# Optimization experiments

Measured on AMD Instinct MI355X. Metric: run time of the kernel, lower is better.

## Reference

```python
import jax, jax.numpy as jnp
import numpy as np

N = 100000        # nodes
E = 1600000       # edges (avg degree 16)
D1, D2 = 512, 256 # omic feature dims
H = 64            # hidden_dim
C = 4             # num_classes


def setup_inputs() -> dict:
    key = jax.random.key(0)
    ks = jax.random.split(key, 13)
    s = 0.05  # param scale
    return {
        "x_omic1": jax.random.normal(ks[0], (N, D1), dtype=jnp.float32),
        "x_omic2": jax.random.normal(ks[1], (N, D2), dtype=jnp.float32),
        "edge_index": jax.random.randint(ks[2], (2, E), 0, N, dtype=jnp.int32),
        # GCNConv weights/biases, branch 1 (omic1)
        "W1a": jax.random.normal(ks[3], (D1, H), dtype=jnp.float32) * s,
        "b1a": jnp.zeros((H,), dtype=jnp.float32),
        "W2a": jax.random.normal(ks[4], (H, H), dtype=jnp.float32) * s,
        "b2a": jnp.zeros((H,), dtype=jnp.float32),
        # branch 2 (omic2)
        "W1b": jax.random.normal(ks[5], (D2, H), dtype=jnp.float32) * s,
        "b1b": jnp.zeros((H,), dtype=jnp.float32),
        "W2b": jax.random.normal(ks[6], (H, H), dtype=jnp.float32) * s,
        "b2b": jnp.zeros((H,), dtype=jnp.float32),
        # final classifier
        "Wfc": jax.random.normal(ks[7], (2 * H, C), dtype=jnp.float32) * s,
        "bfc": jnp.zeros((C,), dtype=jnp.float32),
    }


def reference(x_omic1, x_omic2, edge_index, W1a, b1a, W2a, b2a,
              W1b, b1b, W2b, b2b, Wfc, bfc):
    n = x_omic1.shape[0]
    # GCN normalization with self-loops: A_hat = A + I, norm = d^-1/2 d^-1/2
    loop = jnp.arange(n, dtype=edge_index.dtype)
    src = jnp.concatenate([edge_index[0], loop])
    dst = jnp.concatenate([edge_index[1], loop])
    deg = jax.ops.segment_sum(jnp.ones_like(src, dtype=x_omic1.dtype), dst,
                              num_segments=n)
    dinv = jnp.where(deg > 0, jax.lax.rsqrt(jnp.maximum(deg, 1.0)), 0.0)
    norm = dinv[src] * dinv[dst]  # [E+N]

    def gcn(x, W, b):
        h = x @ W                              # dense linear [n, H]
        msg = h[src] * norm[:, None]           # gather + scale
        return jax.ops.segment_sum(msg, dst, num_segments=n) + b

    # dropout is identity in eval mode
    x1 = jax.nn.elu(gcn(x_omic1, W1a, b1a))
    x1 = jax.nn.elu(gcn(x1, W2a, b2a))
    x2 = jax.nn.elu(gcn(x_omic2, W1b, b1b))
    x2 = jax.nn.elu(gcn(x2, W2b, b2b))
    x = jnp.concatenate([x1, x2], axis=1)      # [n, 2H]
    return x @ Wfc + bfc
```

## Files before the change

kernel.cpp:

```cpp
#include <hip/hip_runtime.h>
#include <hip/hip_bf16.h>
#include <math.h>


#define H 64
#define BCAP 16384

static inline int ceil_div(int a, int b) { return (a + b - 1) / b; }

typedef __attribute__((ext_vector_type(8))) short short8_t;
typedef __attribute__((ext_vector_type(4))) float f32x4;

__device__ inline unsigned short f2bf_rne(float f) {
    unsigned u = __float_as_uint(f);
    u += 0x7fffu + ((u >> 16) & 1u);
    return (unsigned short)(u >> 16);
}
__device__ inline unsigned pk_bf(float a, float b) {
    return (unsigned)f2bf_rne(a) | ((unsigned)f2bf_rne(b) << 16);
}
__device__ inline float2 bf2x(unsigned w) {
    float2 r;
    r.x = __uint_as_float(w << 16);
    r.y = __uint_as_float(w & 0xffff0000u);
    return r;
}
union V8 { uint4 u4; unsigned u[4]; short8_t s; };

__global__ __launch_bounds__(256) void bucket_scatter_kernel(
        const int* __restrict__ src, const int* __restrict__ dst,
        int* __restrict__ cursor, unsigned* __restrict__ bucketed,
        int E, int nbkt) {
    __shared__ int lcnt[512];
    __shared__ int lbase[512];
    const int t = threadIdx.x;
    for (int b = t; b < nbkt; b += 256) lcnt[b] = 0;
    __syncthreads();

    unsigned val[8];
    int bkt[8], lpos[8];
    const int e0 = blockIdx.x * 2048;
#pragma unroll
    for (int k = 0; k < 8; ++k) {
        int e = e0 + k * 256 + t;
        bkt[k] = -1;
        if (e < E) {
            int s = src[e];
            int d = dst[e];
            int b = d >> 8;
            val[k] = (unsigned)s | ((unsigned)(d & 255) << 17);
            bkt[k] = b;
            lpos[k] = atomicAdd(&lcnt[b], 1);
        }
    }
    __syncthreads();
    for (int b = t; b < nbkt; b += 256) {
        int c = lcnt[b];
        lbase[b] = c > 0 ? atomicAdd(&cursor[b], c) : 0;
    }
    __syncthreads();
#pragma unroll
    for (int k = 0; k < 8; ++k) {
        if (bkt[k] >= 0) {
            int p = lbase[bkt[k]] + lpos[k];
            if (p < BCAP)
                bucketed[(size_t)bkt[k] * BCAP + p] = val[k];
        }
    }
}

__global__ __launch_bounds__(256) void bucket_csr_kernel(
        const unsigned* __restrict__ bucketed, const int* __restrict__ cursor,
        int* __restrict__ csr_src, int* __restrict__ row_ptr,
        float* __restrict__ dinv, int N, int E) {
    __shared__ int dcnt[256];
    __shared__ int dbase[256];
    __shared__ int dcur[256];
    const int t = threadIdx.x;
    const int b = blockIdx.x;

    int part = 0;
    for (int i = t; i < b; i += 256) part += cursor[i];
    dbase[t] = part;
    __syncthreads();
#pragma unroll
    for (int off = 128; off > 0; off >>= 1) {
        if (t < off) dbase[t] += dbase[t + off];
        __syncthreads();
    }
    const int base = dbase[0];
    const int cnt = min(cursor[b], BCAP);
    const unsigned* bed = bucketed + (size_t)b * BCAP;
    if (b == 0 && t == 0) row_ptr[N] = E;

    dcnt[t] = 0;
    __syncthreads();
    for (int i = t; i < cnt; i += 256) {
        unsigned v = bed[i];
        atomicAdd(&dcnt[v >> 17], 1);
    }
    __syncthreads();
    int myc = dcnt[t];
    int acc = myc;
    dbase[t] = acc;
    __syncthreads();
#pragma unroll
    for (int off = 1; off < 256; off <<= 1) {
        int u = (t >= off) ? dbase[t - off] : 0;
        __syncthreads();
        dbase[t] += u;
        __syncthreads();
    }
    int excl = dbase[t] - myc;
    dcur[t] = excl;
    int node = b * 256 + t;
    if (node < N) {
        row_ptr[node] = base + excl;
        dinv[node] = rsqrtf((float)myc + 1.0f);
    }
    __syncthreads();
    for (int i = t; i < cnt; i += 256) {
        unsigned v = bed[i];
        int dl = v >> 17;
        int p = atomicAdd(&dcur[dl], 1);
        csr_src[base + p] = (int)(v & 0x1FFFFu);
    }
}

__global__ __launch_bounds__(256) void wfrag4_kernel(
        const float* __restrict__ Wa, uint4* __restrict__ fa,
        const float* __restrict__ Wb, uint4* __restrict__ fb,
        const float* __restrict__ Wc, uint4* __restrict__ fc,
        const float* __restrict__ Wd, uint4* __restrict__ fd,
        int* __restrict__ cursor) {
    const int bid = blockIdx.x;
    if (bid == 0) {
        cursor[threadIdx.x] = 0;
        cursor[threadIdx.x + 256] = 0;
    }
    const float* W;
    uint4* frag;
    int K, t;
    if (bid < 16)      { W = Wa; frag = fa; K = 512; t = bid * 256 + threadIdx.x; }
    else if (bid < 24) { W = Wb; frag = fb; K = 256; t = (bid - 16) * 256 + threadIdx.x; }
    else if (bid < 26) { W = Wc; frag = fc; K = 64;  t = (bid - 24) * 256 + threadIdx.x; }
    else               { W = Wd; frag = fd; K = 64;  t = (bid - 26) * 256 + threadIdx.x; }
    int total = (K >> 5) * 256;
    if (t >= total) return;
    int lane = t & 63, nt = (t >> 6) & 3, ks = t >> 8;
    int nl = lane & 15, q = lane >> 4;
    float hi[8], lo[8];
#pragma unroll
    for (int j = 0; j < 8; ++j) {
        float w = W[(size_t)(ks * 32 + q * 8 + j) * 64 + nt * 16 + nl];
        unsigned hb = f2bf_rne(w);
        float hf = __uint_as_float(((unsigned)hb) << 16);
        hi[j] = hf;
        lo[j] = w - hf;
    }
    V8 vh, vl;
#pragma unroll
    for (int j = 0; j < 4; ++j) {
        vh.u[j] = pk_bf(hi[2 * j], hi[2 * j + 1]);
        vl.u[j] = pk_bf(lo[2 * j], lo[2 * j + 1]);
    }
    size_t base = (size_t)((ks * 4 + nt) * 2) * 64 + lane;
    frag[base] = vh.u4;
    frag[base + 64] = vl.u4;
}

__global__ __launch_bounds__(256) void gemm_l1_kernel(
        const float* __restrict__ XA, const uint4* __restrict__ wfA,
        unsigned* __restrict__ HA, int KA,
        const float* __restrict__ XB, const uint4* __restrict__ wfB,
        unsigned* __restrict__ HB, int KB,
        int M, int nblkA) {
    const float* X;
    const uint4* wf;
    unsigned* Hout;
    int K, blk;
    if ((int)blockIdx.x < nblkA) { X = XA; wf = wfA; Hout = HA; K = KA; blk = blockIdx.x; }
    else                         { X = XB; wf = wfB; Hout = HB; K = KB; blk = blockIdx.x - nblkA; }

    const int tid = threadIdx.x;
    const int w = tid >> 6, l = tid & 63;
    const int m = l & 15, q = l >> 4;
    const int tile = blk * 64 + w * 16;
    int row = tile + m;
    int rowc = row < M ? row : M - 1;
    const float* Xr = X + (size_t)rowc * K;

    f32x4 acc[4];
#pragma unroll
    for (int nt = 0; nt < 4; ++nt) acc[nt] = (f32x4){0.f, 0.f, 0.f, 0.f};

    const int ksteps = K >> 5;
    for (int ks = 0; ks < ksteps; ++ks) {
        const float4 f0 = *(const float4*)&Xr[ks * 32 + q * 8];
        const float4 f1 = *(const float4*)&Xr[ks * 32 + q * 8 + 4];
        float xs[8] = {f0.x, f0.y, f0.z, f0.w, f1.x, f1.y, f1.z, f1.w};
        V8 ah, al;
#pragma unroll
        for (int j = 0; j < 4; ++j) {
            float a = xs[2 * j], b = xs[2 * j + 1];
            unsigned ha = f2bf_rne(a), hb = f2bf_rne(b);
            float fa = __uint_as_float(ha << 16);
            float fb = __uint_as_float(hb << 16);
            ah.u[j] = ha | (hb << 16);
            al.u[j] = pk_bf(a - fa, b - fb);
        }
        const uint4* base = wf + (size_t)(ks * 4) * 2 * 64 + l;
#pragma unroll
        for (int nt = 0; nt < 4; ++nt) {
            V8 bh, bl;
            bh.u4 = base[(size_t)(nt * 2) * 64];
            bl.u4 = base[(size_t)(nt * 2 + 1) * 64];
            acc[nt] = __builtin_amdgcn_mfma_f32_16x16x32_bf16(ah.s, bh.s, acc[nt], 0, 0, 0);
            acc[nt] = __builtin_amdgcn_mfma_f32_16x16x32_bf16(al.s, bh.s, acc[nt], 0, 0, 0);
            acc[nt] = __builtin_amdgcn_mfma_f32_16x16x32_bf16(ah.s, bl.s, acc[nt], 0, 0, 0);
        }
    }

    const int rbase = tile + q * 4;
#pragma unroll
    for (int nt = 0; nt < 4; ++nt) {
#pragma unroll
        for (int i = 0; i < 4; ++i) {
            float f = acc[nt][i];
            float fo = __shfl_xor(f, 1, 64);
            int r = rbase + i;
            if (((l & 1) == 0) && r < M)
                Hout[(size_t)r * 32 + nt * 8 + (m >> 1)] = pk_bf(f, fo);
        }
    }
}

__global__ __launch_bounds__(256) void gemm_l2_kernel(
        const uint4* __restrict__ XA, const uint4* __restrict__ wfA,
        unsigned* __restrict__ HA,
        const uint4* __restrict__ XB, const uint4* __restrict__ wfB,
        unsigned* __restrict__ HB,
        int M, int nblkA) {
    const uint4* Xb;
    const uint4* wf;
    unsigned* Hout;
    int blk;
    if ((int)blockIdx.x < nblkA) { Xb = XA; wf = wfA; Hout = HA; blk = blockIdx.x; }
    else                         { Xb = XB; wf = wfB; Hout = HB; blk = blockIdx.x - nblkA; }

    const int tid = threadIdx.x;
    const int w = tid >> 6, l = tid & 63;
    const int m = l & 15, q = l >> 4;
    const int tile = blk * 64 + w * 16;
    int row = tile + m;
    int rowc = row < M ? row : M - 1;

    f32x4 acc[4];
#pragma unroll
    for (int nt = 0; nt < 4; ++nt) acc[nt] = (f32x4){0.f, 0.f, 0.f, 0.f};

#pragma unroll
    for (int ks = 0; ks < 2; ++ks) {
        V8 av;
        av.u4 = Xb[(size_t)rowc * 8 + ks * 4 + q];
        const uint4* base = wf + (size_t)(ks * 4) * 2 * 64 + l;
#pragma unroll
        for (int nt = 0; nt < 4; ++nt) {
            V8 bh, bl;
            bh.u4 = base[(size_t)(nt * 2) * 64];
            bl.u4 = base[(size_t)(nt * 2 + 1) * 64];
            acc[nt] = __builtin_amdgcn_mfma_f32_16x16x32_bf16(av.s, bh.s, acc[nt], 0, 0, 0);
            acc[nt] = __builtin_amdgcn_mfma_f32_16x16x32_bf16(av.s, bl.s, acc[nt], 0, 0, 0);
        }
    }

    const int rbase = tile + q * 4;
#pragma unroll
    for (int nt = 0; nt < 4; ++nt) {
#pragma unroll
        for (int i = 0; i < 4; ++i) {
            float f = acc[nt][i];
            float fo = __shfl_xor(f, 1, 64);
            int r = rbase + i;
            if (((l & 1) == 0) && r < M)
                Hout[(size_t)r * 32 + nt * 8 + (m >> 1)] = pk_bf(f, fo);
        }
    }
}

__global__ __launch_bounds__(256) void agg2_kernel(const unsigned* __restrict__ h1,
                                                   const unsigned* __restrict__ h2,
                                                   const float* __restrict__ dinv,
                                                   const int* __restrict__ row_ptr,
                                                   const int* __restrict__ csr_src,
                                                   const float* __restrict__ b1,
                                                   const float* __restrict__ b2,
                                                   unsigned* __restrict__ o1,
                                                   unsigned* __restrict__ o2,
                                                   const float* __restrict__ Wfc,
                                                   const float* __restrict__ bfc,
                                                   float* __restrict__ out, int n) {
    const int tid  = threadIdx.x;
    const int lane = tid & 63;
    const int wave = tid >> 6;
    const int half = lane >> 5;
    const int l    = lane & 31;
    const int hb   = half << 5;
    const int node = blockIdx.x * 8 + wave * 2 + half;
    const bool active = (node < n);

    int r0 = 0, r1 = 0;
    float di = 0.f;
    if (active) { r0 = row_ptr[node]; r1 = row_ptr[node + 1]; di = dinv[node]; }
    const float di2 = di * di;
    const int rowoff = node * 32 + l;

    float2 acc1 = make_float2(0.f, 0.f), acc2 = make_float2(0.f, 0.f);
    if (active) {
        float2 s1 = bf2x(h1[rowoff]);
        float2 s2 = bf2x(h2[rowoff]);
        acc1.x = s1.x * di2; acc1.y = s1.y * di2;
        acc2.x = s2.x * di2; acc2.y = s2.y * di2;
    }

    for (int base = r0; base < r1; base += 32) {
        int cnt = r1 - base;
        if (cnt > 32) cnt = 32;
        int j = base + (l < cnt ? l : cnt - 1);
        int sj = csr_src[j];
        float dsj = dinv[sj];
#pragma unroll 4
        for (int t = 0; t < cnt; ++t) {
            int s    = __shfl(sj, hb | t, 64);
            float nr = __shfl(dsj, hb | t, 64) * di;
            float2 g1 = bf2x(h1[s * 32 + l]);
            float2 g2 = bf2x(h2[s * 32 + l]);
            acc1.x = fmaf(g1.x, nr, acc1.x);
            acc1.y = fmaf(g1.y, nr, acc1.y);
            acc2.x = fmaf(g2.x, nr, acc2.x);
            acc2.y = fmaf(g2.y, nr, acc2.y);
        }
    }

    float2 bv1 = ((const float2*)b1)[l];
    float2 bv2 = ((const float2*)b2)[l];
    float2 v1, v2;
    v1.x = acc1.x + bv1.x; v1.y = acc1.y + bv1.y;
    v2.x = acc2.x + bv2.x; v2.y = acc2.y + bv2.y;
    v1.x = v1.x > 0.f ? v1.x : (expf(v1.x) - 1.f);
    v1.y = v1.y > 0.f ? v1.y : (expf(v1.y) - 1.f);
    v2.x = v2.x > 0.f ? v2.x : (expf(v2.x) - 1.f);
    v2.y = v2.y > 0.f ? v2.y : (expf(v2.y) - 1.f);

    if (Wfc == nullptr) {
        if (active) {
            o1[rowoff] = pk_bf(v1.x, v1.y);
            o2[rowoff] = pk_bf(v2.x, v2.y);
        }
        return;
    }

    const float* Wp1 = &Wfc[(2 * l) * 4];
    const float* Wp2 = &Wfc[(H + 2 * l) * 4];
    float a[4];
#pragma unroll
    for (int c = 0; c < 4; ++c)
        a[c] = v1.x * Wp1[c] + v1.y * Wp1[4 + c] + v2.x * Wp2[c] + v2.y * Wp2[4 + c];
#pragma unroll
    for (int off = 16; off > 0; off >>= 1) {
#pragma unroll
        for (int c = 0; c < 4; ++c)
            a[c] += __shfl_down(a[c], off, 64);
    }
    if (l == 0 && active) {
#pragma unroll
        for (int c = 0; c < 4; ++c)
            out[(size_t)node * 4 + c] = a[c] + bfc[c];
    }
}

extern "C" void kernel_launch(void* const* d_in, const int* in_sizes, int n_in,
                              void* d_out, int out_size, void* d_ws, size_t ws_size,
                              hipStream_t stream) {
    const float* x_omic1 = (const float*)d_in[0];
    const float* x_omic2 = (const float*)d_in[1];
    const int*   eidx    = (const int*)d_in[2];
    const float* W1a = (const float*)d_in[3];
    const float* b1a = (const float*)d_in[4];
    const float* W2a = (const float*)d_in[5];
    const float* b2a = (const float*)d_in[6];
    const float* W1b = (const float*)d_in[7];
    const float* b1b = (const float*)d_in[8];
    const float* W2b = (const float*)d_in[9];
    const float* b2b = (const float*)d_in[10];
    const float* Wfc = (const float*)d_in[11];
    const float* bfc = (const float*)d_in[12];
    float* out = (float*)d_out;

    const int D1 = 512, D2 = 256;
    const int N = in_sizes[0] / D1;
    const int E = in_sizes[2] / 2;
    const int* src = eidx;
    const int* dst = eidx + E;
    const int nbkt = ceil_div(N, 256);

    size_t off = 0;
    auto alloc = [&](size_t elems) { size_t o = off; off += (elems + 3) & ~(size_t)3; return o; };
    float*    base_f = (float*)d_ws;
    int*      base_i = (int*)d_ws;
    unsigned* base_u = (unsigned*)d_ws;
    float*    dinv     = base_f + alloc(N);
    int*      row_ptr  = base_i + alloc(N + 1);
    int*      cursor   = base_i + alloc(512);
    unsigned* bucketed = base_u + alloc((size_t)nbkt * BCAP);
    int*      csr_src  = base_i + alloc(E);
    unsigned* h1bf     = base_u + alloc((size_t)N * 32);
    unsigned* h2bf     = base_u + alloc((size_t)N * 32);
    unsigned* x1bf     = base_u + alloc((size_t)N * 32);
    unsigned* x2bf     = base_u + alloc((size_t)N * 32);
    uint4*    wf1a = (uint4*)(base_u + alloc((D1 / 32) * 2 * 256 * 4));
    uint4*    wf1b = (uint4*)(base_u + alloc((D2 / 32) * 2 * 256 * 4));
    uint4*    wf2a = (uint4*)(base_u + alloc((H  / 32) * 2 * 256 * 4));
    uint4*    wf2b = (uint4*)(base_u + alloc((H  / 32) * 2 * 256 * 4));

    dim3 blk(256);
    dim3 grid_agg(ceil_div(N, 8));
    const int nblk = ceil_div(N, 64);

    wfrag4_kernel<<<28, blk, 0, stream>>>(W1a, wf1a, W1b, wf1b, W2a, wf2a,
                                          W2b, wf2b, cursor);
    bucket_scatter_kernel<<<ceil_div(E, 2048), blk, 0, stream>>>(src, dst, cursor,
                                                                 bucketed, E, nbkt);
    bucket_csr_kernel<<<nbkt, blk, 0, stream>>>(bucketed, cursor, csr_src,
                                                row_ptr, dinv, N, E);
    gemm_l1_kernel<<<2 * nblk, blk, 0, stream>>>(x_omic1, wf1a, h1bf, D1,
                                                 x_omic2, wf1b, h2bf, D2, N, nblk);
    agg2_kernel<<<grid_agg, blk, 0, stream>>>(h1bf, h2bf, dinv, row_ptr, csr_src,
                                              b1a, b1b, x1bf, x2bf,
                                              nullptr, nullptr, nullptr, N);
    gemm_l2_kernel<<<2 * nblk, blk, 0, stream>>>((const uint4*)x1bf, wf2a, h1bf,
                                                 (const uint4*)x2bf, wf2b, h2bf,
                                                 N, nblk);
    agg2_kernel<<<grid_agg, blk, 0, stream>>>(h1bf, h2bf, dinv, row_ptr, csr_src,
                                              b2a, b2b, nullptr, nullptr,
                                              Wfc, bfc, out, N);
}
```

Measured before the change: 699.4 us.

## Compute four 16-row subtiles per wave in layer-1 GEMM to reuse weight fragments

Each wave of the first-layer GEMM now handles 64 rows (four 16-row subtiles) instead of 16. The weight fragments for a k-step are loaded once and reused across all four subtiles, and the grid shrinks fourfold. This cuts repeated weight loads and raises memory-level parallelism per wave, since more X loads are in flight at once. The cost is higher register pressure (64 accumulator floats plus staged inputs) and fewer blocks, which may lower occupancy on a kernel that is largely bound by streaming X from memory.

```diff
diff --git a/kernel.cpp b/kernel.cpp
--- a/kernel.cpp
+++ b/kernel.cpp
@@ -185,52 +185,76 @@
     const int tid = threadIdx.x;
     const int w = tid >> 6, l = tid & 63;
     const int m = l & 15, q = l >> 4;
-    const int tile = blk * 64 + w * 16;
-    int row = tile + m;
-    int rowc = row < M ? row : M - 1;
-    const float* Xr = X + (size_t)rowc * K;
-
-    f32x4 acc[4];
-#pragma unroll
-    for (int nt = 0; nt < 4; ++nt) acc[nt] = (f32x4){0.f, 0.f, 0.f, 0.f};
+    const int wbase = blk * 256 + w * 64;
+
+    const float* Xr[4];
+#pragma unroll
+    for (int s = 0; s < 4; ++s) {
+        int row = wbase + s * 16 + m;
+        int rowc = row < M ? row : M - 1;
+        Xr[s] = X + (size_t)rowc * K;
+    }
+
+    f32x4 acc[4][4];
+#pragma unroll
+    for (int s = 0; s < 4; ++s)
+#pragma unroll
+        for (int nt = 0; nt < 4; ++nt) acc[s][nt] = (f32x4){0.f, 0.f, 0.f, 0.f};
 
     const int ksteps = K >> 5;
     for (int ks = 0; ks < ksteps; ++ks) {
-        const float4 f0 = *(const float4*)&Xr[ks * 32 + q * 8];
-        const float4 f1 = *(const float4*)&Xr[ks * 32 + q * 8 + 4];
-        float xs[8] = {f0.x, f0.y, f0.z, f0.w, f1.x, f1.y, f1.z, f1.w};
-        V8 ah, al;
-#pragma unroll
-        for (int j = 0; j < 4; ++j) {
-            float a = xs[2 * j], b = xs[2 * j + 1];
-            unsigned ha = f2bf_rne(a), hb = f2bf_rne(b);
-            float fa = __uint_as_float(ha << 16);
-            float fb = __uint_as_float(hb << 16);
-            ah.u[j] = ha | (hb << 16);
-            al.u[j] = pk_bf(a - fa, b - fb);
+        float4 xf[4][2];
+#pragma unroll
+        for (int s = 0; s < 4; ++s) {
+            xf[s][0] = *(const float4*)&Xr[s][ks * 32 + q * 8];
+            xf[s][1] = *(const float4*)&Xr[s][ks * 32 + q * 8 + 4];
         }
         const uint4* base = wf + (size_t)(ks * 4) * 2 * 64 + l;
+        uint4 bh[4], bl[4];
 #pragma unroll
         for (int nt = 0; nt < 4; ++nt) {
-            V8 bh, bl;
-            bh.u4 = base[(size_t)(nt * 2) * 64];
-            bl.u4 = base[(size_t)(nt * 2 + 1) * 64];
-            acc[nt] = __builtin_amdgcn_mfma_f32_16x16x32_bf16(ah.s, bh.s, acc[nt], 0, 0, 0);
-            acc[nt] = __builtin_amdgcn_mfma_f32_16x16x32_bf16(al.s, bh.s, acc[nt], 0, 0, 0);
-            acc[nt] = __builtin_amdgcn_mfma_f32_16x16x32_bf16(ah.s, bl.s, acc[nt], 0, 0, 0);
-        }
-    }
-
-    const int rbase = tile + q * 4;
-#pragma unroll
-    for (int nt = 0; nt < 4; ++nt) {
-#pragma unroll
-        for (int i = 0; i < 4; ++i) {
-            float f = acc[nt][i];
-            float fo = __shfl_xor(f, 1, 64);
-            int r = rbase + i;
-            if (((l & 1) == 0) && r < M)
-                Hout[(size_t)r * 32 + nt * 8 + (m >> 1)] = pk_bf(f, fo);
+            bh[nt] = base[(size_t)(nt * 2) * 64];
+            bl[nt] = base[(size_t)(nt * 2 + 1) * 64];
+        }
+#pragma unroll
+        for (int s = 0; s < 4; ++s) {
+            float xs[8] = {xf[s][0].x, xf[s][0].y, xf[s][0].z, xf[s][0].w,
+                           xf[s][1].x, xf[s][1].y, xf[s][1].z, xf[s][1].w};
+            V8 ah, al;
+#pragma unroll
+            for (int j = 0; j < 4; ++j) {
+                float a = xs[2 * j], b = xs[2 * j + 1];
+                unsigned ha = f2bf_rne(a), hb = f2bf_rne(b);
+                float fa = __uint_as_float(ha << 16);
+                float fb = __uint_as_float(hb << 16);
+                ah.u[j] = ha | (hb << 16);
+                al.u[j] = pk_bf(a - fa, b - fb);
+            }
+#pragma unroll
+            for (int nt = 0; nt < 4; ++nt) {
+                V8 vh, vl;
+                vh.u4 = bh[nt];
+                vl.u4 = bl[nt];
+                acc[s][nt] = __builtin_amdgcn_mfma_f32_16x16x32_bf16(ah.s, vh.s, acc[s][nt], 0, 0, 0);
+                acc[s][nt] = __builtin_amdgcn_mfma_f32_16x16x32_bf16(al.s, vh.s, acc[s][nt], 0, 0, 0);
+                acc[s][nt] = __builtin_amdgcn_mfma_f32_16x16x32_bf16(ah.s, vl.s, acc[s][nt], 0, 0, 0);
+            }
+        }
+    }
+
+#pragma unroll
+    for (int s = 0; s < 4; ++s) {
+        const int rbase = wbase + s * 16 + q * 4;
+#pragma unroll
+        for (int nt = 0; nt < 4; ++nt) {
+#pragma unroll
+            for (int i = 0; i < 4; ++i) {
+                float f = acc[s][nt][i];
+                float fo = __shfl_xor(f, 1, 64);
+                int r = rbase + i;
+                if (((l & 1) == 0) && r < M)
+                    Hout[(size_t)r * 32 + nt * 8 + (m >> 1)] = pk_bf(f, fo);
+            }
         }
     }
 }
@@ -426,6 +450,7 @@
     dim3 blk(256);
     dim3 grid_agg(ceil_div(N, 8));
     const int nblk = ceil_div(N, 64);
+    const int nblkL1 = ceil_div(N, 256);
 
     wfrag4_kernel<<<28, blk, 0, stream>>>(W1a, wf1a, W1b, wf1b, W2a, wf2a,
                                           W2b, wf2b, cursor);
@@ -433,8 +458,8 @@
                                                                  bucketed, E, nbkt);
     bucket_csr_kernel<<<nbkt, blk, 0, stream>>>(bucketed, cursor, csr_src,
                                                 row_ptr, dinv, N, E);
-    gemm_l1_kernel<<<2 * nblk, blk, 0, stream>>>(x_omic1, wf1a, h1bf, D1,
-                                                 x_omic2, wf1b, h2bf, D2, N, nblk);
+    gemm_l1_kernel<<<2 * nblkL1, blk, 0, stream>>>(x_omic1, wf1a, h1bf, D1,
+                                                   x_omic2, wf1b, h2bf, D2, N, nblkL1);
     agg2_kernel<<<grid_agg, blk, 0, stream>>>(h1bf, h2bf, dinv, row_ptr, csr_src,
                                               b1a, b1b, x1bf, x2bf,
                                               nullptr, nullptr, nullptr, N);
```

After: 687.0 us. Within noise of the previous version (-1.8%).
